# Optimization experiments

Measured on AMD Instinct MI355X. Metric: run time of the kernel, lower is better.

The kernel has to match this reference:

```python
import jax, jax.numpy as jnp
import numpy as np


def _conv(x, w, b, stride, pad):
    # x: [N,C,H,W], w: [O,I,kh,kw]
    y = jax.lax.conv_general_dilated(
        x, w, (stride, stride), [(pad, pad), (pad, pad)],
        dimension_numbers=('NCHW', 'OIHW', 'NCHW'))
    return y + b[None, :, None, None]


def _block(x, w1, b1, w2, b2, stride):
    # BasicBlock with BN folded: conv3x3 -> relu -> conv3x3
    h = jax.nn.relu(_conv(x, w1, b1, stride, 1))
    return _conv(h, w2, b2, 1, 1)


def setup_inputs() -> dict:
    key = jax.random.key(0)
    keys = iter(jax.random.split(key, 64))

    def rn(shape):
        fan_in = int(np.prod(shape[1:])) if len(shape) > 1 else shape[0]
        return jax.random.normal(next(keys), shape, jnp.float32) * (1.0 / np.sqrt(fan_in))

    d = {}
    d['inputs'] = jax.random.normal(next(keys), (128, 3, 64, 64), jnp.float32)
    d['probs'] = jax.random.uniform(next(keys), (128, 15), jnp.float32)
    d['seed_w'] = rn((64, 3, 3, 3))
    d['seed_b'] = jnp.zeros((64,), jnp.float32)
    specs = [(64, 64), (64, 128), (128, 256)]  # (cin, cout) per group
    for g, (ci, co) in enumerate(specs):
        d[f'g{g}_ds_w'] = rn((co, ci, 1, 1))
        d[f'g{g}_ds_b'] = jnp.zeros((co,), jnp.float32)
        d[f'g{g}_b0_w1'] = rn((co, ci, 3, 3))
        d[f'g{g}_b0_b1'] = jnp.zeros((co,), jnp.float32)
        d[f'g{g}_b0_w2'] = rn((co, co, 3, 3))
        d[f'g{g}_b0_b2'] = jnp.zeros((co,), jnp.float32)
        d[f'g{g}_r_w1'] = rn((4, co, co, 3, 3))
        d[f'g{g}_r_b1'] = jnp.zeros((4, co), jnp.float32)
        d[f'g{g}_r_w2'] = rn((4, co, co, 3, 3))
        d[f'g{g}_r_b2'] = jnp.zeros((4, co), jnp.float32)
    d['fc_w'] = rn((1000, 256))
    d['fc_b'] = jnp.zeros((1000,), jnp.float32)
    return d


def reference(inputs, probs, seed_w, seed_b,
              g0_ds_w, g0_ds_b, g0_b0_w1, g0_b0_b1, g0_b0_w2, g0_b0_b2,
              g0_r_w1, g0_r_b1, g0_r_w2, g0_r_b2,
              g1_ds_w, g1_ds_b, g1_b0_w1, g1_b0_b1, g1_b0_w2, g1_b0_b2,
              g1_r_w1, g1_r_b1, g1_r_w2, g1_r_b2,
              g2_ds_w, g2_ds_b, g2_b0_w1, g2_b0_b1, g2_b0_w2, g2_b0_b2,
              g2_r_w1, g2_r_b1, g2_r_w2, g2_r_b2,
              fc_w, fc_b):
    # policy[k, n] in {0,1}: hard-threshold of agent probs at 0.5 (forward_real)
    policy = jnp.where(probs < 0.5, 0.0, 1.0).astype(inputs.dtype).T  # [15, B]
    x = jax.nn.relu(_conv(inputs, seed_w, seed_b, 1, 1))
    groups = [
        (g0_ds_w, g0_ds_b, g0_b0_w1, g0_b0_b1, g0_b0_w2, g0_b0_b2, g0_r_w1, g0_r_b1, g0_r_w2, g0_r_b2, 1),
        (g1_ds_w, g1_ds_b, g1_b0_w1, g1_b0_b1, g1_b0_w2, g1_b0_b2, g1_r_w1, g1_r_b1, g1_r_w2, g1_r_b2, 2),
        (g2_ds_w, g2_ds_b, g2_b0_w1, g2_b0_b1, g2_b0_w2, g2_b0_b2, g2_r_w1, g2_r_b1, g2_r_w2, g2_r_b2, 2),
    ]
    idx = 0
    for (ds_w, ds_b, b0_w1, b0_b1, b0_w2, b0_b2, r_w1, r_b1, r_w2, r_b2, s) in groups:
        # first block of the group: strided, with 1x1 downsample residual
        residual = _conv(x, ds_w, ds_b, s, 0)
        fx = _block(x, b0_w1, b0_b1, b0_w2, b0_b2, s)
        m = policy[idx][:, None, None, None]
        idx += 1
        x = m * jax.nn.relu(residual + fx) + (1.0 - m) * residual
        # remaining 4 identity-residual blocks
        for j in range(4):
            residual = x
            fx = _block(x, r_w1[j], r_b1[j], r_w2[j], r_b2[j], 1)
            m = policy[idx][:, None, None, None]
            idx += 1
            x = m * jax.nn.relu(residual + fx) + (1.0 - m) * residual
    pooled = x.mean(axis=(2, 3))  # global average pool [B, 256]
    return pooled @ fc_w.T + fc_b
```

## Files before the change

### kernel.cpp

```cpp
#include <hip/hip_runtime.h>

using bf = unsigned short;
typedef __attribute__((ext_vector_type(8))) short short8v;
typedef __attribute__((ext_vector_type(4))) float f32x4;
typedef __attribute__((ext_vector_type(4))) unsigned int u32x4;
typedef __attribute__((ext_vector_type(2))) unsigned int u32x2;

__device__ __forceinline__ float bf2f(bf u) { return __uint_as_float(((unsigned)u) << 16); }
__device__ __forceinline__ bf f2bf(float f) {
    unsigned x = __float_as_uint(f);
    x += 0x7fffu + ((x >> 16) & 1u);
    return (bf)(x >> 16);
}

template <int CC, int RS, int STRIDE, bool RELU, bool COMBINE, int LOG2W>
__global__ __launch_bounds__(256) void conv_mfma(
    const bf* __restrict__ X, const bf* __restrict__ Wp,
    const float* __restrict__ bias, bf* __restrict__ Y,
    const bf* __restrict__ res, const float* __restrict__ probs,
    int kidx, int Ci, int Co) {
    constexpr int W = 1 << LOG2W;
    constexpr int ROWS = 128 >> LOG2W;
    constexpr int PAD = (RS == 3) ? 1 : 0;
    constexpr int IN_ROWS = (ROWS - 1) * STRIDE + RS;
    constexpr int IN_COLS = (W - 1) * STRIDE + RS;
    constexpr int NG = CC / 8;
    constexpr int HIN = W * STRIDE;
    constexpr int RSRS = RS * RS;

    __shared__ bf sX[IN_ROWS * IN_COLS * CC];

    const int tid = threadIdx.x;
    const int n = blockIdx.z;
    const int coBase = blockIdx.y << 6;
    const int r0 = blockIdx.x * ROWS;
    const size_t pixBase = (size_t)n * W * W + (size_t)r0 * W;

    bool active = true;
    if (kidx >= 0) active = (probs[n * 15 + kidx] >= 0.5f);
    if (!active) {
        if constexpr (COMBINE) {
            for (int i = tid; i < (128 * 64) / 8; i += 256) {
                int lp = i >> 3;
                int c8 = (i & 7) * 8;
                size_t off = (pixBase + lp) * Co + coBase + c8;
                u32x4 v = *reinterpret_cast<const u32x4*>(res + off);
                *reinterpret_cast<u32x4*>(Y + off) = v;
            }
        }
        return;
    }

    const int lane = tid & 63;
    const int wid = tid >> 6;
    const int l15 = lane & 15;
    const int lq = lane >> 4;
    const int wm = wid >> 1;
    const int wn = wid & 1;

    f32x4 acc[2][4] = {};

    int prow[4], pcol[4];
#pragma unroll
    for (int nf = 0; nf < 4; ++nf) {
        int p = wn * 64 + nf * 16 + l15;
        prow[nf] = p >> LOG2W;
        pcol[nf] = p & (W - 1);
    }

    const bf* Xn = X + (size_t)n * HIN * HIN * Ci;
    const int NCH = Ci / CC;

    for (int ch = 0; ch < NCH; ++ch) {
        if (ch) __syncthreads();
        constexpr int TG = IN_ROWS * IN_COLS * NG;
        for (int g = tid; g < TG; g += 256) {
            int ir = g / (IN_COLS * NG);
            int rem = g - ir * (IN_COLS * NG);
            int ic = rem / NG;
            int gc = rem - ic * NG;
            int in_r = r0 * STRIDE - PAD + ir;
            int in_c = ic - PAD;
            u32x4 v = {0, 0, 0, 0};
            if ((unsigned)in_r < (unsigned)HIN && (unsigned)in_c < (unsigned)HIN) {
                v = *reinterpret_cast<const u32x4*>(
                    Xn + ((size_t)in_r * HIN + in_c) * Ci + ch * CC + gc * 8);
            }
            int gsw = gc ^ (ic & (NG - 1));
            *reinterpret_cast<u32x4*>(&sX[((ir * IN_COLS + ic) * NG + gsw) * 8]) = v;
        }
        __syncthreads();

        if constexpr (CC >= 32) {
#pragma unroll
            for (int j = 0; j < RSRS; ++j) {
                const int dh = j / RS;
                const int dw = j % RS;
#pragma unroll
                for (int kk = 0; kk < CC / 32; ++kk) {
                    short8v a[2];
#pragma unroll
                    for (int mf = 0; mf < 2; ++mf) {
                        int co = coBase + wm * 32 + mf * 16 + l15;
                        a[mf] = *reinterpret_cast<const short8v*>(
                            Wp + (((size_t)(ch * RSRS + j) * Co + co) * CC + kk * 32 + lq * 8));
                    }
                    short8v b[4];
#pragma unroll
                    for (int nf = 0; nf < 4; ++nf) {
                        int ir = prow[nf] * STRIDE + dh;
                        int ic = pcol[nf] * STRIDE + dw;
                        int gk = (kk * 4 + lq) ^ (ic & (NG - 1));
                        b[nf] = *reinterpret_cast<const short8v*>(
                            &sX[((ir * IN_COLS + ic) * NG + gk) * 8]);
                    }
#pragma unroll
                    for (int mf = 0; mf < 2; ++mf)
#pragma unroll
                        for (int nf = 0; nf < 4; ++nf)
                            acc[mf][nf] = __builtin_amdgcn_mfma_f32_16x16x32_bf16(
                                a[mf], b[nf], acc[mf][nf], 0, 0, 0);
                }
            }
        } else {
#pragma unroll
            for (int kt = 0; kt < 3; ++kt) {
                int j = kt * 4 + lq;
                int jj = (j < 9) ? j : 0;
                int dh = jj / 3, dw = jj % 3;
                short8v a[2];
#pragma unroll
                for (int mf = 0; mf < 2; ++mf) {
                    int co = coBase + wm * 32 + mf * 16 + l15;
                    a[mf] = *reinterpret_cast<const short8v*>(Wp + ((size_t)j * Co + co) * 8);
                }
                short8v b[4];
#pragma unroll
                for (int nf = 0; nf < 4; ++nf) {
                    int ir = prow[nf] + dh;
                    int ic = pcol[nf] + dw;
                    b[nf] = *reinterpret_cast<const short8v*>(&sX[(ir * IN_COLS + ic) * 8]);
                }
#pragma unroll
                for (int mf = 0; mf < 2; ++mf)
#pragma unroll
                    for (int nf = 0; nf < 4; ++nf)
                        acc[mf][nf] = __builtin_amdgcn_mfma_f32_16x16x32_bf16(
                            a[mf], b[nf], acc[mf][nf], 0, 0, 0);
            }
        }
    }

#pragma unroll
    for (int mf = 0; mf < 2; ++mf) {
        int co0 = coBase + wm * 32 + mf * 16 + lq * 4;
        float4 b4 = *reinterpret_cast<const float4*>(bias + co0);
        float bb[4] = {b4.x, b4.y, b4.z, b4.w};
#pragma unroll
        for (int nf = 0; nf < 4; ++nf) {
            int p = wn * 64 + nf * 16 + l15;
            size_t off = (pixBase + p) * Co + co0;
            float v[4];
#pragma unroll
            for (int i = 0; i < 4; ++i) v[i] = acc[mf][nf][i] + bb[i];
            if constexpr (COMBINE) {
                u32x2 r2 = *reinterpret_cast<const u32x2*>(res + off);
                bf rr[4] = {(bf)(r2[0] & 0xffff), (bf)(r2[0] >> 16),
                            (bf)(r2[1] & 0xffff), (bf)(r2[1] >> 16)};
#pragma unroll
                for (int i = 0; i < 4; ++i) v[i] = fmaxf(v[i] + bf2f(rr[i]), 0.f);
            }
            if constexpr (RELU) {
#pragma unroll
                for (int i = 0; i < 4; ++i) v[i] = fmaxf(v[i], 0.f);
            }
            unsigned lo = (unsigned)f2bf(v[0]) | ((unsigned)f2bf(v[1]) << 16);
            unsigned hi = (unsigned)f2bf(v[2]) | ((unsigned)f2bf(v[3]) << 16);
            u32x2 o2 = {lo, hi};
            *reinterpret_cast<u32x2*>(Y + off) = o2;
        }
    }
}

__global__ void repack_k(const float* __restrict__ w, bf* __restrict__ wp,
                         int Co, int Ci, int RSRS, int CC, int JPAD, size_t total) {
    size_t idx = (size_t)blockIdx.x * 256 + threadIdx.x;
    if (idx >= total) return;
    int cw = (int)(idx % CC);
    int co = (int)((idx / CC) % Co);
    int j = (int)((idx / ((size_t)CC * Co)) % JPAD);
    int ch = (int)(idx / ((size_t)CC * Co * JPAD));
    int ci = ch * CC + cw;
    float v = 0.f;
    if (ci < Ci && j < RSRS) v = w[((size_t)co * Ci + ci) * RSRS + j];
    wp[idx] = f2bf(v);
}

__global__ void cvt_in(const float* __restrict__ in, bf* __restrict__ out) {
    size_t idx = (size_t)blockIdx.x * 256 + threadIdx.x;
    int c = (int)(idx & 7);
    size_t pix = idx >> 3;
    int w = (int)(pix & 63);
    int h = (int)((pix >> 6) & 63);
    int n = (int)(pix >> 12);
    float v = 0.f;
    if (c < 3) v = in[(((size_t)n * 3 + c) * 64 + h) * 64 + w];
    out[idx] = f2bf(v);
}

__global__ void pool_k(const bf* __restrict__ X, float* __restrict__ pooled) {
    int n = blockIdx.x;
    int co = threadIdx.x;
    float s = 0.f;
    for (int p = 0; p < 256; ++p) s += bf2f(X[((size_t)n * 256 + p) * 256 + co]);
    pooled[n * 256 + co] = s * (1.f / 256.f);
}

__global__ void fc_k(const float* __restrict__ pooled, const float* __restrict__ fw,
                     const float* __restrict__ fb, float* __restrict__ out) {
    __shared__ float sp[256];
    int n = blockIdx.x;
    sp[threadIdx.x] = pooled[n * 256 + threadIdx.x];
    __syncthreads();
    for (int o = threadIdx.x; o < 1000; o += 256) {
        float acc = fb[o];
        for (int k = 0; k < 256; ++k) acc += sp[k] * fw[(size_t)o * 256 + k];
        out[(size_t)n * 1000 + o] = acc;
    }
}

template <int S, int LW, int CC1>
static void run_group(hipStream_t st, bf* X, bf* H, bf* OUT,
                      bf* wp_ds, const float* ds_b, bf* wp_w1, const float* b1,
                      bf* wp_w2, const float* b2, bf* const* wp_rw1, const float* rb1,
                      bf* const* wp_rw2, const float* rb2, const float* probs_c,
                      int kbase, int Ci, int Co, int NB) {
    constexpr int Wo = 1 << LW;
    dim3 grid((Wo * Wo) / 128, Co / 64, NB);
    conv_mfma<64, 1, S, false, false, LW><<<grid, 256, 0, st>>>(
        X, wp_ds, ds_b, OUT, nullptr, nullptr, -1, Ci, Co);
    conv_mfma<CC1, 3, S, true, false, LW><<<grid, 256, 0, st>>>(
        X, wp_w1, b1, H, nullptr, probs_c, kbase, Ci, Co);
    conv_mfma<64, 3, 1, false, true, LW><<<grid, 256, 0, st>>>(
        H, wp_w2, b2, OUT, OUT, probs_c, kbase, Co, Co);
    for (int j = 0; j < 4; ++j) {
        conv_mfma<64, 3, 1, true, false, LW><<<grid, 256, 0, st>>>(
            OUT, wp_rw1[j], rb1 + j * Co, H, nullptr, probs_c, kbase + 1 + j, Co, Co);
        conv_mfma<64, 3, 1, false, true, LW><<<grid, 256, 0, st>>>(
            H, wp_rw2[j], rb2 + j * Co, OUT, OUT, probs_c, kbase + 1 + j, Co, Co);
    }
}

extern "C" void kernel_launch(void* const* d_in, const int* in_sizes, int n_in,
                              void* d_out, int out_size, void* d_ws, size_t ws_size,
                              hipStream_t stream) {
    const float* input = (const float*)d_in[0];
    const float* probs = (const float*)d_in[1];
    const float* seed_w = (const float*)d_in[2];
    const float* seed_b = (const float*)d_in[3];
    const float* fc_w = (const float*)d_in[34];
    const float* fc_b = (const float*)d_in[35];

    char* pw = (char*)d_ws;
    auto alloc = [&](size_t bytes) -> void* {
        void* r = (void*)pw;
        pw += ((bytes + 255) & ~(size_t)255);
        return r;
    };

    bf* xin = (bf*)alloc(128ull * 64 * 64 * 8 * 2);
    float* pooled = (float*)alloc(128 * 256 * 4);

    auto pack = [&](const float* w, int Co_, int Ci_, int RSRS_, int CC_, int JPAD_) -> bf* {
        int NCH_ = (Ci_ + CC_ - 1) / CC_;
        size_t total = (size_t)NCH_ * JPAD_ * Co_ * CC_;
        bf* wp = (bf*)alloc(total * 2);
        repack_k<<<dim3((unsigned)((total + 255) / 256)), 256, 0, stream>>>(
            w, wp, Co_, Ci_, RSRS_, CC_, JPAD_, total);
        return wp;
    };

    cvt_in<<<dim3(16384), 256, 0, stream>>>(input, xin);

    bf* wpSeed = pack(seed_w, 64, 3, 9, 8, 12);
    const int cis[3] = {64, 64, 128};
    const int cos[3] = {64, 128, 256};
    const int cc1s[3] = {64, 32, 32};
    bf* wp_ds[3];
    bf* wp_w1[3];
    bf* wp_w2[3];
    bf* wp_rw1[3][4];
    bf* wp_rw2[3][4];
    const float *ds_b[3], *b1[3], *b2[3], *rb1[3], *rb2[3];
    for (int g = 0; g < 3; ++g) {
        int base = 4 + g * 10;
        const float* dsw = (const float*)d_in[base + 0];
        ds_b[g] = (const float*)d_in[base + 1];
        const float* w1 = (const float*)d_in[base + 2];
        b1[g] = (const float*)d_in[base + 3];
        const float* w2 = (const float*)d_in[base + 4];
        b2[g] = (const float*)d_in[base + 5];
        const float* rw1 = (const float*)d_in[base + 6];
        rb1[g] = (const float*)d_in[base + 7];
        const float* rw2 = (const float*)d_in[base + 8];
        rb2[g] = (const float*)d_in[base + 9];
        int Ci = cis[g], Co = cos[g];
        wp_ds[g] = pack(dsw, Co, Ci, 1, 64, 1);
        wp_w1[g] = pack(w1, Co, Ci, 9, cc1s[g], 9);
        wp_w2[g] = pack(w2, Co, Co, 9, 64, 9);
        for (int j = 0; j < 4; ++j) {
            wp_rw1[g][j] = pack(rw1 + (size_t)j * Co * Co * 9, Co, Co, 9, 64, 9);
            wp_rw2[g][j] = pack(rw2 + (size_t)j * Co * Co * 9, Co, Co, 9, 64, 9);
        }
    }

    size_t used = (size_t)(pw - (char*)d_ws);
    size_t avail = (ws_size > used) ? (ws_size - used) : 0;
    const size_t PER_IMG = 64ull * 64 * 64 * 2;
    int NB = 128;
    while (NB > 8 && (size_t)3 * NB * PER_IMG + 4096 > avail) NB >>= 1;

    bf* A = (bf*)alloc((size_t)NB * PER_IMG);
    bf* Bb = (bf*)alloc((size_t)NB * PER_IMG);
    bf* C = (bf*)alloc((size_t)NB * PER_IMG);

    for (int n0 = 0; n0 < 128; n0 += NB) {
        const float* pc = probs + (size_t)n0 * 15;
        conv_mfma<8, 3, 1, true, false, 6><<<dim3(32, 1, NB), 256, 0, stream>>>(
            xin + (size_t)n0 * 64 * 64 * 8, wpSeed, seed_b, A, nullptr, nullptr, -1, 8, 64);

        run_group<1, 6, 64>(stream, A, Bb, C, wp_ds[0], ds_b[0], wp_w1[0], b1[0],
                            wp_w2[0], b2[0], wp_rw1[0], rb1[0], wp_rw2[0], rb2[0],
                            pc, 0, 64, 64, NB);
        run_group<2, 5, 32>(stream, C, Bb, A, wp_ds[1], ds_b[1], wp_w1[1], b1[1],
                            wp_w2[1], b2[1], wp_rw1[1], rb1[1], wp_rw2[1], rb2[1],
                            pc, 5, 64, 128, NB);
        run_group<2, 4, 32>(stream, A, Bb, C, wp_ds[2], ds_b[2], wp_w1[2], b1[2],
                            wp_w2[2], b2[2], wp_rw1[2], rb1[2], wp_rw2[2], rb2[2],
                            pc, 10, 128, 256, NB);

        pool_k<<<dim3(NB), 256, 0, stream>>>(C, pooled + (size_t)n0 * 256);
    }

    fc_k<<<dim3(128), 256, 0, stream>>>(pooled, fc_w, fc_b, (float*)d_out);
}
```

Baseline: 2.261 ms.

## Use 512-thread conv blocks, register prefetch, direct 1x1 path, batched repack, vectorized pool

Conv blocks now run 8 waves of 512 threads, each wave computing a 32x32 tile instead of 64x32, with launch bounds asking for 4 blocks per CU to hide latency. Input channels become a compile-time template parameter. The 1x1 downsample conv reads global memory directly without shared-memory staging. Multi-chunk 3x3 convs prefetch the next channel chunk into registers while computing the current one. All weight repacks are merged into a single launch, and pooling is vectorized across 8 slices. The cost is higher register pressure and less operand reuse per wave.

```diff
diff --git a/kernel.cpp b/kernel.cpp
--- a/kernel.cpp
+++ b/kernel.cpp
@@ -13,12 +13,12 @@
     return (bf)(x >> 16);
 }
 
-template <int CC, int RS, int STRIDE, bool RELU, bool COMBINE, int LOG2W>
-__global__ __launch_bounds__(256) void conv_mfma(
+template <int CI, int CC, int RS, int STRIDE, bool RELU, bool COMBINE, int LOG2W>
+__global__ __launch_bounds__(512, 4) void conv_mfma(
     const bf* __restrict__ X, const bf* __restrict__ Wp,
     const float* __restrict__ bias, bf* __restrict__ Y,
     const bf* __restrict__ res, const float* __restrict__ probs,
-    int kidx, int Ci, int Co) {
+    int kidx, int Co) {
     constexpr int W = 1 << LOG2W;
     constexpr int ROWS = 128 >> LOG2W;
     constexpr int PAD = (RS == 3) ? 1 : 0;
@@ -27,8 +27,13 @@
     constexpr int NG = CC / 8;
     constexpr int HIN = W * STRIDE;
     constexpr int RSRS = RS * RS;
-
-    __shared__ bf sX[IN_ROWS * IN_COLS * CC];
+    constexpr int NCH = CI / CC;
+    constexpr bool DIRECT = (RS == 1);
+    constexpr int TG = IN_ROWS * IN_COLS * NG;
+    constexpr int NITER = (TG + 511) / 512;
+    constexpr bool PREF = (!DIRECT) && (CC == 64) && (NCH > 1);
+
+    __shared__ bf sX[DIRECT ? 1 : IN_ROWS * IN_COLS * CC];
 
     const int tid = threadIdx.x;
     const int n = blockIdx.z;
@@ -40,10 +45,8 @@
     if (kidx >= 0) active = (probs[n * 15 + kidx] >= 0.5f);
     if (!active) {
         if constexpr (COMBINE) {
-            for (int i = tid; i < (128 * 64) / 8; i += 256) {
-                int lp = i >> 3;
-                int c8 = (i & 7) * 8;
-                size_t off = (pixBase + lp) * Co + coBase + c8;
+            for (int i = tid; i < (128 * 64) / 8; i += 512) {
+                size_t off = (pixBase + (i >> 3)) * Co + coBase + (i & 7) * 8;
                 u32x4 v = *reinterpret_cast<const u32x4*>(res + off);
                 *reinterpret_cast<u32x4*>(Y + off) = v;
             }
@@ -55,98 +58,181 @@
     const int wid = tid >> 6;
     const int l15 = lane & 15;
     const int lq = lane >> 4;
-    const int wm = wid >> 1;
-    const int wn = wid & 1;
-
-    f32x4 acc[2][4] = {};
-
-    int prow[4], pcol[4];
-#pragma unroll
-    for (int nf = 0; nf < 4; ++nf) {
-        int p = wn * 64 + nf * 16 + l15;
+    const int wm = wid >> 2;
+    const int wn = wid & 3;
+
+    f32x4 acc[2][2] = {};
+    int prow[2], pcol[2];
+#pragma unroll
+    for (int nf = 0; nf < 2; ++nf) {
+        int p = wn * 32 + nf * 16 + l15;
         prow[nf] = p >> LOG2W;
         pcol[nf] = p & (W - 1);
     }
 
-    const bf* Xn = X + (size_t)n * HIN * HIN * Ci;
-    const int NCH = Ci / CC;
-
-    for (int ch = 0; ch < NCH; ++ch) {
-        if (ch) __syncthreads();
-        constexpr int TG = IN_ROWS * IN_COLS * NG;
-        for (int g = tid; g < TG; g += 256) {
-            int ir = g / (IN_COLS * NG);
-            int rem = g - ir * (IN_COLS * NG);
-            int ic = rem / NG;
-            int gc = rem - ic * NG;
-            int in_r = r0 * STRIDE - PAD + ir;
-            int in_c = ic - PAD;
-            u32x4 v = {0, 0, 0, 0};
-            if ((unsigned)in_r < (unsigned)HIN && (unsigned)in_c < (unsigned)HIN) {
-                v = *reinterpret_cast<const u32x4*>(
-                    Xn + ((size_t)in_r * HIN + in_c) * Ci + ch * CC + gc * 8);
-            }
-            int gsw = gc ^ (ic & (NG - 1));
-            *reinterpret_cast<u32x4*>(&sX[((ir * IN_COLS + ic) * NG + gsw) * 8]) = v;
-        }
-        __syncthreads();
-
-        if constexpr (CC >= 32) {
-#pragma unroll
-            for (int j = 0; j < RSRS; ++j) {
-                const int dh = j / RS;
-                const int dw = j % RS;
-#pragma unroll
-                for (int kk = 0; kk < CC / 32; ++kk) {
-                    short8v a[2];
+    const bf* Xn = X + (size_t)n * HIN * HIN * CI;
+
+    if constexpr (DIRECT) {
+#pragma unroll
+        for (int ch = 0; ch < NCH; ++ch) {
+#pragma unroll
+            for (int kk = 0; kk < CC / 32; ++kk) {
+                short8v a[2], b[2];
+#pragma unroll
+                for (int mf = 0; mf < 2; ++mf) {
+                    int co = coBase + wm * 32 + mf * 16 + l15;
+                    a[mf] = *reinterpret_cast<const short8v*>(
+                        Wp + ((size_t)ch * Co + co) * CC + kk * 32 + lq * 8);
+                }
+#pragma unroll
+                for (int nf = 0; nf < 2; ++nf) {
+                    b[nf] = *reinterpret_cast<const short8v*>(
+                        Xn + ((size_t)((r0 + prow[nf]) * STRIDE) * HIN + pcol[nf] * STRIDE) * CI +
+                        ch * CC + kk * 32 + lq * 8);
+                }
+#pragma unroll
+                for (int mf = 0; mf < 2; ++mf)
+#pragma unroll
+                    for (int nf = 0; nf < 2; ++nf)
+                        acc[mf][nf] = __builtin_amdgcn_mfma_f32_16x16x32_bf16(
+                            a[mf], b[nf], acc[mf][nf], 0, 0, 0);
+            }
+        }
+    } else {
+        auto stage = [&](int ch) {
+#pragma unroll
+            for (int i = 0; i < NITER; ++i) {
+                int g = tid + i * 512;
+                bool inb = (TG % 512 == 0) ? true : (g < TG);
+                if (inb) {
+                    int ir = g / (IN_COLS * NG);
+                    int rem = g - ir * (IN_COLS * NG);
+                    int ic = rem / NG;
+                    int gc = rem - ic * NG;
+                    int in_r = r0 * STRIDE - PAD + ir;
+                    int in_c = ic - PAD;
+                    u32x4 v = {0, 0, 0, 0};
+                    if ((unsigned)in_r < (unsigned)HIN && (unsigned)in_c < (unsigned)HIN)
+                        v = *reinterpret_cast<const u32x4*>(
+                            Xn + ((size_t)in_r * HIN + in_c) * CI + ch * CC + gc * 8);
+                    int gsw = gc ^ (ic & (NG - 1));
+                    *reinterpret_cast<u32x4*>(&sX[((ir * IN_COLS + ic) * NG + gsw) * 8]) = v;
+                }
+            }
+        };
+
+        auto compute = [&](int ch) {
+            if constexpr (CC >= 32) {
+#pragma unroll
+                for (int j = 0; j < RSRS; ++j) {
+                    const int dh = j / RS;
+                    const int dw = j % RS;
+#pragma unroll
+                    for (int kk = 0; kk < CC / 32; ++kk) {
+                        short8v a[2], b[2];
+#pragma unroll
+                        for (int mf = 0; mf < 2; ++mf) {
+                            int co = coBase + wm * 32 + mf * 16 + l15;
+                            a[mf] = *reinterpret_cast<const short8v*>(
+                                Wp + (((size_t)(ch * RSRS + j) * Co + co) * CC + kk * 32 + lq * 8));
+                        }
+#pragma unroll
+                        for (int nf = 0; nf < 2; ++nf) {
+                            int ir = prow[nf] * STRIDE + dh;
+                            int ic = pcol[nf] * STRIDE + dw;
+                            int gk = (kk * 4 + lq) ^ (ic & (NG - 1));
+                            b[nf] = *reinterpret_cast<const short8v*>(
+                                &sX[((ir * IN_COLS + ic) * NG + gk) * 8]);
+                        }
+#pragma unroll
+                        for (int mf = 0; mf < 2; ++mf)
+#pragma unroll
+                            for (int nf = 0; nf < 2; ++nf)
+                                acc[mf][nf] = __builtin_amdgcn_mfma_f32_16x16x32_bf16(
+                                    a[mf], b[nf], acc[mf][nf], 0, 0, 0);
+                    }
+                }
+            } else {
+#pragma unroll
+                for (int kt = 0; kt < 3; ++kt) {
+                    int j = kt * 4 + lq;
+                    int jj = (j < 9) ? j : 0;
+                    int dh = jj / 3, dw = jj % 3;
+                    short8v a[2], b[2];
 #pragma unroll
                     for (int mf = 0; mf < 2; ++mf) {
                         int co = coBase + wm * 32 + mf * 16 + l15;
-                        a[mf] = *reinterpret_cast<const short8v*>(
-                            Wp + (((size_t)(ch * RSRS + j) * Co + co) * CC + kk * 32 + lq * 8));
+                        a[mf] = *reinterpret_cast<const short8v*>(Wp + ((size_t)j * Co + co) * 8);
                     }
-                    short8v b[4];
-#pragma unroll
-                    for (int nf = 0; nf < 4; ++nf) {
-                        int ir = prow[nf] * STRIDE + dh;
-                        int ic = pcol[nf] * STRIDE + dw;
-                        int gk = (kk * 4 + lq) ^ (ic & (NG - 1));
-                        b[nf] = *reinterpret_cast<const short8v*>(
-                            &sX[((ir * IN_COLS + ic) * NG + gk) * 8]);
+#pragma unroll
+                    for (int nf = 0; nf < 2; ++nf) {
+                        int ir = prow[nf] + dh;
+                        int ic = pcol[nf] + dw;
+                        b[nf] = *reinterpret_cast<const short8v*>(&sX[(ir * IN_COLS + ic) * 8]);
                     }
 #pragma unroll
                     for (int mf = 0; mf < 2; ++mf)
 #pragma unroll
-                        for (int nf = 0; nf < 4; ++nf)
+                        for (int nf = 0; nf < 2; ++nf)
                             acc[mf][nf] = __builtin_amdgcn_mfma_f32_16x16x32_bf16(
                                 a[mf], b[nf], acc[mf][nf], 0, 0, 0);
                 }
             }
+        };
+
+        if constexpr (PREF) {
+            u32x4 pf[NITER];
+            stage(0);
+            __syncthreads();
+#pragma unroll
+            for (int ch = 0; ch < NCH; ++ch) {
+                if (ch + 1 < NCH) {
+#pragma unroll
+                    for (int i = 0; i < NITER; ++i) {
+                        int g = tid + i * 512;
+                        bool inb = (TG % 512 == 0) ? true : (g < TG);
+                        u32x4 v = {0, 0, 0, 0};
+                        if (inb) {
+                            int ir = g / (IN_COLS * NG);
+                            int rem = g - ir * (IN_COLS * NG);
+                            int ic = rem / NG;
+                            int gc = rem - ic * NG;
+                            int in_r = r0 * STRIDE - PAD + ir;
+                            int in_c = ic - PAD;
+                            if ((unsigned)in_r < (unsigned)HIN && (unsigned)in_c < (unsigned)HIN)
+                                v = *reinterpret_cast<const u32x4*>(
+                                    Xn + ((size_t)in_r * HIN + in_c) * CI + (ch + 1) * CC + gc * 8);
+                        }
+                        pf[i] = v;
+                    }
+                }
+                compute(ch);
+                if (ch + 1 < NCH) {
+                    __syncthreads();
+#pragma unroll
+                    for (int i = 0; i < NITER; ++i) {
+                        int g = tid + i * 512;
+                        bool inb = (TG % 512 == 0) ? true : (g < TG);
+                        if (inb) {
+                            int ir = g / (IN_COLS * NG);
+                            int rem = g - ir * (IN_COLS * NG);
+                            int ic = rem / NG;
+                            int gc = rem - ic * NG;
+                            int gsw = gc ^ (ic & (NG - 1));
+                            *reinterpret_cast<u32x4*>(
+                                &sX[((ir * IN_COLS + ic) * NG + gsw) * 8]) = pf[i];
+                        }
+                    }
+                    __syncthreads();
+                }
+            }
         } else {
 #pragma unroll
-            for (int kt = 0; kt < 3; ++kt) {
-                int j = kt * 4 + lq;
-                int jj = (j < 9) ? j : 0;
-                int dh = jj / 3, dw = jj % 3;
-                short8v a[2];
-#pragma unroll
-                for (int mf = 0; mf < 2; ++mf) {
-                    int co = coBase + wm * 32 + mf * 16 + l15;
-                    a[mf] = *reinterpret_cast<const short8v*>(Wp + ((size_t)j * Co + co) * 8);
-                }
-                short8v b[4];
-#pragma unroll
-                for (int nf = 0; nf < 4; ++nf) {
-                    int ir = prow[nf] + dh;
-                    int ic = pcol[nf] + dw;
-                    b[nf] = *reinterpret_cast<const short8v*>(&sX[(ir * IN_COLS + ic) * 8]);
-                }
-#pragma unroll
-                for (int mf = 0; mf < 2; ++mf)
-#pragma unroll
-                    for (int nf = 0; nf < 4; ++nf)
-                        acc[mf][nf] = __builtin_amdgcn_mfma_f32_16x16x32_bf16(
-                            a[mf], b[nf], acc[mf][nf], 0, 0, 0);
+            for (int ch = 0; ch < NCH; ++ch) {
+                if (ch) __syncthreads();
+                stage(ch);
+                __syncthreads();
+                compute(ch);
             }
         }
     }
@@ -157,8 +243,8 @@
         float4 b4 = *reinterpret_cast<const float4*>(bias + co0);
         float bb[4] = {b4.x, b4.y, b4.z, b4.w};
 #pragma unroll
-        for (int nf = 0; nf < 4; ++nf) {
-            int p = wn * 64 + nf * 16 + l15;
+        for (int nf = 0; nf < 2; ++nf) {
+            int p = wn * 32 + nf * 16 + l15;
             size_t off = (pixBase + p) * Co + co0;
             float v[4];
 #pragma unroll
@@ -182,18 +268,34 @@
     }
 }
 
-__global__ void repack_k(const float* __restrict__ w, bf* __restrict__ wp,
-                         int Co, int Ci, int RSRS, int CC, int JPAD, size_t total) {
-    size_t idx = (size_t)blockIdx.x * 256 + threadIdx.x;
+#define NSEG 34
+struct Seg {
+    const float* src;
+    bf* dst;
+    int Co, Ci, RSRS, CC, JPAD, blk0;
+};
+struct SegArgs {
+    Seg s[NSEG];
+};
+__global__ void repack_all(SegArgs A) {
+    int b = blockIdx.x;
+    int lo = 0;
+#pragma unroll 1
+    for (int i = 1; i < NSEG; ++i)
+        if (A.s[i].blk0 <= b) lo = i;
+    Seg sg = A.s[lo];
+    int NCH_ = (sg.Ci + sg.CC - 1) / sg.CC;
+    size_t total = (size_t)NCH_ * sg.JPAD * sg.Co * sg.CC;
+    size_t idx = (size_t)(b - sg.blk0) * 256 + threadIdx.x;
     if (idx >= total) return;
-    int cw = (int)(idx % CC);
-    int co = (int)((idx / CC) % Co);
-    int j = (int)((idx / ((size_t)CC * Co)) % JPAD);
-    int ch = (int)(idx / ((size_t)CC * Co * JPAD));
-    int ci = ch * CC + cw;
+    int cw = (int)(idx % sg.CC);
+    int co = (int)((idx / sg.CC) % sg.Co);
+    int j = (int)((idx / ((size_t)sg.CC * sg.Co)) % sg.JPAD);
+    int ch = (int)(idx / ((size_t)sg.CC * sg.Co * sg.JPAD));
+    int ci = ch * sg.CC + cw;
     float v = 0.f;
-    if (ci < Ci && j < RSRS) v = w[((size_t)co * Ci + ci) * RSRS + j];
-    wp[idx] = f2bf(v);
+    if (ci < sg.Ci && j < sg.RSRS) v = sg.src[((size_t)co * sg.Ci + ci) * sg.RSRS + j];
+    sg.dst[idx] = f2bf(v);
 }
 
 __global__ void cvt_in(const float* __restrict__ in, bf* __restrict__ out) {
@@ -209,11 +311,31 @@
 }
 
 __global__ void pool_k(const bf* __restrict__ X, float* __restrict__ pooled) {
+    __shared__ float red[8][256];
     int n = blockIdx.x;
-    int co = threadIdx.x;
-    float s = 0.f;
-    for (int p = 0; p < 256; ++p) s += bf2f(X[((size_t)n * 256 + p) * 256 + co]);
-    pooled[n * 256 + co] = s * (1.f / 256.f);
+    int g = threadIdx.x & 31;
+    int slice = threadIdx.x >> 5;
+    float acc[8] = {};
+    for (int p = slice * 32; p < slice * 32 + 32; ++p) {
+        u32x4 v = *reinterpret_cast<const u32x4*>(X + ((size_t)n * 256 + p) * 256 + g * 8);
+#pragma unroll
+        for (int i = 0; i < 4; ++i) {
+            acc[2 * i] += bf2f((bf)(v[i] & 0xffff));
+            acc[2 * i + 1] += bf2f((bf)(v[i] >> 16));
+        }
+    }
+#pragma unroll
+    for (int i = 0; i < 8; ++i) red[slice][g * 8 + i] = acc[i];
+    __syncthreads();
+    if (slice == 0) {
+#pragma unroll
+        for (int i = 0; i < 8; ++i) {
+            float s = 0.f;
+#pragma unroll
+            for (int ss = 0; ss < 8; ++ss) s += red[ss][g * 8 + i];
+            pooled[n * 256 + g * 8 + i] = s * (1.f / 256.f);
+        }
+    }
 }
 
 __global__ void fc_k(const float* __restrict__ pooled, const float* __restrict__ fw,
@@ -229,31 +351,32 @@
     }
 }
 
-template <int S, int LW, int CC1>
+template <int CIN, int COUT, int S, int LW, int CC1>
 static void run_group(hipStream_t st, bf* X, bf* H, bf* OUT,
                       bf* wp_ds, const float* ds_b, bf* wp_w1, const float* b1,
                       bf* wp_w2, const float* b2, bf* const* wp_rw1, const float* rb1,
                       bf* const* wp_rw2, const float* rb2, const float* probs_c,
-                      int kbase, int Ci, int Co, int NB) {
+                      int kbase, int NB) {
     constexpr int Wo = 1 << LW;
-    dim3 grid((Wo * Wo) / 128, Co / 64, NB);
-    conv_mfma<64, 1, S, false, false, LW><<<grid, 256, 0, st>>>(
-        X, wp_ds, ds_b, OUT, nullptr, nullptr, -1, Ci, Co);
-    conv_mfma<CC1, 3, S, true, false, LW><<<grid, 256, 0, st>>>(
-        X, wp_w1, b1, H, nullptr, probs_c, kbase, Ci, Co);
-    conv_mfma<64, 3, 1, false, true, LW><<<grid, 256, 0, st>>>(
-        H, wp_w2, b2, OUT, OUT, probs_c, kbase, Co, Co);
+    dim3 grid((Wo * Wo) / 128, COUT / 64, NB);
+    conv_mfma<CIN, 64, 1, S, false, false, LW><<<grid, 512, 0, st>>>(
+        X, wp_ds, ds_b, OUT, nullptr, nullptr, -1, COUT);
+    conv_mfma<CIN, CC1, 3, S, true, false, LW><<<grid, 512, 0, st>>>(
+        X, wp_w1, b1, H, nullptr, probs_c, kbase, COUT);
+    conv_mfma<COUT, 64, 3, 1, false, true, LW><<<grid, 512, 0, st>>>(
+        H, wp_w2, b2, OUT, OUT, probs_c, kbase, COUT);
     for (int j = 0; j < 4; ++j) {
-        conv_mfma<64, 3, 1, true, false, LW><<<grid, 256, 0, st>>>(
-            OUT, wp_rw1[j], rb1 + j * Co, H, nullptr, probs_c, kbase + 1 + j, Co, Co);
-        conv_mfma<64, 3, 1, false, true, LW><<<grid, 256, 0, st>>>(
-            H, wp_rw2[j], rb2 + j * Co, OUT, OUT, probs_c, kbase + 1 + j, Co, Co);
+        conv_mfma<COUT, 64, 3, 1, true, false, LW><<<grid, 512, 0, st>>>(
+            OUT, wp_rw1[j], rb1 + j * COUT, H, nullptr, probs_c, kbase + 1 + j, COUT);
+        conv_mfma<COUT, 64, 3, 1, false, true, LW><<<grid, 512, 0, st>>>(
+            H, wp_rw2[j], rb2 + j * COUT, OUT, OUT, probs_c, kbase + 1 + j, COUT);
     }
 }
 
 extern "C" void kernel_launch(void* const* d_in, const int* in_sizes, int n_in,
                               void* d_out, int out_size, void* d_ws, size_t ws_size,
                               hipStream_t stream) {
+    (void)in_sizes; (void)n_in; (void)out_size;
     const float* input = (const float*)d_in[0];
     const float* probs = (const float*)d_in[1];
     const float* seed_w = (const float*)d_in[2];
@@ -271,12 +394,16 @@
     bf* xin = (bf*)alloc(128ull * 64 * 64 * 8 * 2);
     float* pooled = (float*)alloc(128 * 256 * 4);
 
+    SegArgs sa;
+    int nseg = 0;
+    int blkAcc = 0;
     auto pack = [&](const float* w, int Co_, int Ci_, int RSRS_, int CC_, int JPAD_) -> bf* {
         int NCH_ = (Ci_ + CC_ - 1) / CC_;
         size_t total = (size_t)NCH_ * JPAD_ * Co_ * CC_;
         bf* wp = (bf*)alloc(total * 2);
-        repack_k<<<dim3((unsigned)((total + 255) / 256)), 256, 0, stream>>>(
-            w, wp, Co_, Ci_, RSRS_, CC_, JPAD_, total);
+        sa.s[nseg] = {w, wp, Co_, Ci_, RSRS_, CC_, JPAD_, blkAcc};
+        blkAcc += (int)((total + 255) / 256);
+        ++nseg;
         return wp;
     };
 
@@ -313,6 +440,8 @@
             wp_rw2[g][j] = pack(rw2 + (size_t)j * Co * Co * 9, Co, Co, 9, 64, 9);
         }
     }
+    for (int i = nseg; i < NSEG; ++i) sa.s[i] = {nullptr, nullptr, 1, 1, 1, 1, 1, 0x7fffffff};
+    repack_all<<<dim3(blkAcc), 256, 0, stream>>>(sa);
 
     size_t used = (size_t)(pw - (char*)d_ws);
     size_t avail = (ws_size > used) ? (ws_size - used) : 0;
@@ -326,18 +455,18 @@
 
     for (int n0 = 0; n0 < 128; n0 += NB) {
         const float* pc = probs + (size_t)n0 * 15;
-        conv_mfma<8, 3, 1, true, false, 6><<<dim3(32, 1, NB), 256, 0, stream>>>(
-            xin + (size_t)n0 * 64 * 64 * 8, wpSeed, seed_b, A, nullptr, nullptr, -1, 8, 64);
-
-        run_group<1, 6, 64>(stream, A, Bb, C, wp_ds[0], ds_b[0], wp_w1[0], b1[0],
-                            wp_w2[0], b2[0], wp_rw1[0], rb1[0], wp_rw2[0], rb2[0],
-                            pc, 0, 64, 64, NB);
-        run_group<2, 5, 32>(stream, C, Bb, A, wp_ds[1], ds_b[1], wp_w1[1], b1[1],
-                            wp_w2[1], b2[1], wp_rw1[1], rb1[1], wp_rw2[1], rb2[1],
-                            pc, 5, 64, 128, NB);
-        run_group<2, 4, 32>(stream, A, Bb, C, wp_ds[2], ds_b[2], wp_w1[2], b1[2],
-                            wp_w2[2], b2[2], wp_rw1[2], rb1[2], wp_rw2[2], rb2[2],
-                            pc, 10, 128, 256, NB);
+        conv_mfma<8, 8, 3, 1, true, false, 6><<<dim3(32, 1, NB), 512, 0, stream>>>(
+            xin + (size_t)n0 * 64 * 64 * 8, wpSeed, seed_b, A, nullptr, nullptr, -1, 64);
+
+        run_group<64, 64, 1, 6, 64>(stream, A, Bb, C, wp_ds[0], ds_b[0], wp_w1[0], b1[0],
+                                    wp_w2[0], b2[0], wp_rw1[0], rb1[0], wp_rw2[0], rb2[0],
+                                    pc, 0, NB);
+        run_group<64, 128, 2, 5, 32>(stream, C, Bb, A, wp_ds[1], ds_b[1], wp_w1[1], b1[1],
+                                     wp_w2[1], b2[1], wp_rw1[1], rb1[1], wp_rw2[1], rb2[1],
+                                     pc, 5, NB);
+        run_group<128, 256, 2, 4, 32>(stream, A, Bb, C, wp_ds[2], ds_b[2], wp_w1[2], b1[2],
+                                      wp_w2[2], b2[2], wp_rw1[2], rb1[2], wp_rw2[2], rb2[2],
+                                      pc, 10, NB);
 
         pool_k<<<dim3(NB), 256, 0, stream>>>(C, pooled + (size_t)n0 * 256);
     }
```

After: 3.184 ms. +40.9%, slower.
